# Kernel tuning notes

Measured on AMD Instinct MI355X. Metric: run time of the kernel, lower is better.

Reference implementation:

```python
import jax, jax.numpy as jnp
import numpy as np

H = 768       # hidden size
NH = 12       # num attention heads
DH = H // NH  # head dim = 64
B = 32
S = 512


def setup_inputs() -> dict:
    key = jax.random.key(0)
    ks = jax.random.split(key, 7)
    scale = 1.0 / np.sqrt(H)
    return {
        "inputs": jax.random.normal(ks[0], (B, S, H), dtype=jnp.float32),
        "Wq": jax.random.normal(ks[1], (H, H), dtype=jnp.float32) * scale,
        "bq": jnp.zeros((H,), dtype=jnp.float32),
        "Wk": jax.random.normal(ks[2], (H, H), dtype=jnp.float32) * scale,
        "bk": jnp.zeros((H,), dtype=jnp.float32),
        "Wv": jax.random.normal(ks[3], (H, H), dtype=jnp.float32) * scale,
        "bv": jnp.zeros((H,), dtype=jnp.float32),
    }


def reference(inputs, Wq, bq, Wk, bk, Wv, bv):
    # BertSelfAttention: linear projections (torch Linear: x @ W.T + b)
    def split_heads(x):  # [B,S,H] -> [B,NH,S,DH]
        return x.reshape(B, S, NH, DH).transpose(0, 2, 1, 3)

    q = split_heads(inputs @ Wq.T + bq)
    k = split_heads(inputs @ Wk.T + bk)
    v = split_heads(inputs @ Wv.T + bv)

    # scores [B,NH,S,S]; the wrapper adds an all-zero attention mask (no-op)
    scores = jnp.einsum("bhqd,bhkd->bhqk", q, k) / jnp.sqrt(jnp.float32(DH))
    probs = jax.nn.softmax(scores, axis=-1)
    ctx = jnp.einsum("bhqk,bhkd->bhqd", probs, v)  # [B,NH,S,DH]
    ctx = ctx.transpose(0, 2, 1, 3).reshape(B, S, H)
    return jnp.tanh(ctx)
```

## Files before the change

kernel.cpp:

```cpp
#include <hip/hip_runtime.h>
#include <hip/hip_bf16.h>
#include <cmath>

#define Bc   32
#define Sc_  512
#define Hc   768
#define NHc  12
#define DHc  64
#define Mc   (Bc * Sc_)
#define Ntot (3 * Hc)

#define QSCALE 0.18033688011112042f

typedef __attribute__((ext_vector_type(8))) short short8v;
typedef __attribute__((ext_vector_type(8))) unsigned short ushort8v;
typedef __attribute__((ext_vector_type(4))) float f32x4;

static __device__ __forceinline__ ushort f2b(float f) {
    __hip_bfloat16 h = __float2bfloat16(f);
    return *reinterpret_cast<ushort*>(&h);
}

static __device__ __forceinline__ void gl2lds(const ushort* g, ushort* l) {
    __builtin_amdgcn_global_load_lds(
        (const __attribute__((address_space(1))) unsigned int*)g,
        (__attribute__((address_space(3))) unsigned int*)l, 16, 0, 0);
}

static __device__ __forceinline__ float fast_tanh(float x) {
    float e = __builtin_amdgcn_exp2f(x * 2.885390081777927f);
    return 1.0f - 2.0f * __builtin_amdgcn_rcpf(e + 1.0f);
}

#define NXC (Mc * 96)
#define NWC (Ntot * 96)
__global__ __launch_bounds__(256) void convert_pack(
    const float* __restrict__ X,
    const float* __restrict__ Wq, const float* __restrict__ Wk,
    const float* __restrict__ Wv,
    const float* __restrict__ bq, const float* __restrict__ bk,
    const float* __restrict__ bv,
    ushort* __restrict__ Xt, ushort* __restrict__ Wt, float* __restrict__ bbp)
{
    int tid = blockIdx.x * 256 + threadIdx.x;
    if (tid < NXC) {
        int kc   = tid % 96;
        int m    = tid / 96;
        int mblk = m >> 7, mrow = m & 127;
        const float* src = X + (size_t)m * Hc + kc * 8;
        float4 f0 = *(const float4*)&src[0];
        float4 f1 = *(const float4*)&src[4];
        ushort8v o;
        o[0] = f2b(f0.x); o[1] = f2b(f0.y); o[2] = f2b(f0.z); o[3] = f2b(f0.w);
        o[4] = f2b(f1.x); o[5] = f2b(f1.y); o[6] = f2b(f1.z); o[7] = f2b(f1.w);
        *(ushort8v*)&Xt[((size_t)(mblk * 96 + kc)) * 1024 + mrow * 8] = o;
    } else if (tid < NXC + NWC) {
        int t2 = tid - NXC;
        int kc   = t2 % 96;
        int n    = t2 / 96;
        int nblk = n >> 7, nrow = n & 127;
        int z = n / Hc, nn = n - z * Hc;
        const float* W = (z == 0) ? Wq : (z == 1) ? Wk : Wv;
        const float* src = W + (size_t)nn * Hc + kc * 8;
        float4 f0 = *(const float4*)&src[0];
        float4 f1 = *(const float4*)&src[4];
        ushort8v o;
        o[0] = f2b(f0.x); o[1] = f2b(f0.y); o[2] = f2b(f0.z); o[3] = f2b(f0.w);
        o[4] = f2b(f1.x); o[5] = f2b(f1.y); o[6] = f2b(f1.z); o[7] = f2b(f1.w);
        *(ushort8v*)&Wt[((size_t)(nblk * 96 + kc)) * 1024 + nrow * 8] = o;
    } else if (tid < NXC + NWC + Ntot) {
        int i = tid - NXC - NWC;
        int z = i / Hc, nn = i - z * Hc;
        bbp[i] = ((z == 0) ? bq : (z == 1) ? bk : bv)[nn];
    }
}

__global__ __launch_bounds__(256) void qkv_mfma(
    const ushort* __restrict__ Xt, const ushort* __restrict__ Wt,
    const float* __restrict__ bbp,
    ushort* __restrict__ Qb, ushort* __restrict__ Kt, ushort* __restrict__ Vt)
{
    const int tid = threadIdx.x;
    const int wave = tid >> 6, lane = tid & 63;
    const int quad = lane >> 4, l16 = lane & 15;
    const int wr = wave >> 1, wc = wave & 1;
    const int m0 = blockIdx.x * 128;
    const int n0 = blockIdx.y * 128;

    __shared__ __align__(16) ushort As[4096];
    __shared__ __align__(16) ushort Bs[4096];

    f32x4 acc[4][4];
    #pragma unroll
    for (int i = 0; i < 4; ++i)
        #pragma unroll
        for (int j = 0; j < 4; ++j) acc[i][j] = (f32x4)(0.f);

    const ushort* gA = Xt + (size_t)blockIdx.x * (96 * 1024) + wave * 1024 + lane * 8;
    const ushort* gB = Wt + (size_t)blockIdx.y * (96 * 1024) + wave * 1024 + lane * 8;
    ushort* lA = As + wave * 1024;
    ushort* lB = Bs + wave * 1024;

    for (int t = 0; t < 24; ++t) {
        const ushort* ga = gA + t * 4096;
        const ushort* gb = gB + t * 4096;
        gl2lds(ga,       lA);
        gl2lds(ga + 512, lA + 512);
        gl2lds(gb,       lB);
        gl2lds(gb + 512, lB + 512);
        __syncthreads();

        short8v a[4], b[4];
        #pragma unroll
        for (int i = 0; i < 4; ++i)
            a[i] = *(const short8v*)&As[quad * 1024 + (wr * 64 + i * 16 + l16) * 8];
        #pragma unroll
        for (int j = 0; j < 4; ++j)
            b[j] = *(const short8v*)&Bs[quad * 1024 + (wc * 64 + j * 16 + l16) * 8];
        #pragma unroll
        for (int i = 0; i < 4; ++i)
            #pragma unroll
            for (int j = 0; j < 4; ++j)
                acc[i][j] = __builtin_amdgcn_mfma_f32_16x16x32_bf16(
                    a[i], b[j], acc[i][j], 0, 0, 0);
        __syncthreads();
    }

    const int z = n0 / Hc;
    #pragma unroll
    for (int j = 0; j < 4; ++j) {
        const int n  = n0 + wc * 64 + j * 16 + l16;
        const int nn = n - z * Hc;
        const int h  = nn >> 6, d = nn & 63;
        const float bias = bbp[n];
        #pragma unroll
        for (int i = 0; i < 4; ++i) {
            const int mbase = m0 + wr * 64 + i * 16 + quad * 4;
            const int bb = mbase >> 9;
            const int s0 = mbase & 511;
            const size_t head = (size_t)(bb * NHc + h) * (Sc_ * DHc);
            if (z == 0) {
                size_t base = head + (size_t)s0 * DHc + d;
                #pragma unroll
                for (int r = 0; r < 4; ++r)
                    Qb[base + (size_t)r * DHc] = f2b((acc[i][j][r] + bias) * QSCALE);
            } else if (z == 1) {
                size_t base = head + (s0 >> 6) * 4096 + (d >> 3) * 512
                            + (s0 & 63) * 8 + (d & 7);
                #pragma unroll
                for (int r = 0; r < 4; ++r)
                    Kt[base + r * 8] = f2b(acc[i][j][r] + bias);
            } else {
                size_t base = head + (s0 >> 6) * 4096 + ((s0 & 63) >> 3) * 512
                            + d * 8 + (s0 & 7);
                ushort4 o;
                o.x = f2b(acc[i][j][0] + bias);
                o.y = f2b(acc[i][j][1] + bias);
                o.z = f2b(acc[i][j][2] + bias);
                o.w = f2b(acc[i][j][3] + bias);
                *(ushort4*)&Vt[base] = o;
            }
        }
    }
}

__global__ __launch_bounds__(256) void attn_mfma(
    const ushort* __restrict__ Qb, const ushort* __restrict__ Kt,
    const ushort* __restrict__ Vt, float* __restrict__ out)
{
    const int b = blockIdx.z, h = blockIdx.y;
    const int wave = threadIdx.x >> 6;
    const int lane = threadIdx.x & 63;
    const int quad = lane >> 4, l16 = lane & 15;
    const int q0 = blockIdx.x * 128 + wave * 32;
    const int sw = l16 & 7;

    const size_t head = (size_t)(b * NHc + h) * (Sc_ * DHc);
    const ushort* __restrict__ Q = Qb + head;
    const ushort* __restrict__ K = Kt + head;
    const ushort* __restrict__ V = Vt + head;

    __shared__ __align__(16) ushort Plds[4][2][1024];

    short8v aq[2][2];
    #pragma unroll
    for (int u = 0; u < 2; ++u)
        #pragma unroll
        for (int hf = 0; hf < 2; ++hf)
            aq[u][hf] = *(const short8v*)
                &Q[(size_t)(q0 + u * 16 + l16) * DHc + hf * 32 + quad * 8];

    f32x4 o[2][4];
    #pragma unroll
    for (int u = 0; u < 2; ++u)
        #pragma unroll
        for (int t = 0; t < 4; ++t) o[u][t] = (f32x4)(0.f);
    float rs[2] = {0.f, 0.f};

    for (int kb = 0; kb < 8; ++kb) {
        const ushort* Kb_ = K + kb * 4096;
        const ushort* Vb_ = V + kb * 4096;

        short8v kf[4][2];
        #pragma unroll
        for (int t = 0; t < 4; ++t) {
            kf[t][0] = *(const short8v*)&Kb_[quad * 512 + (t * 16 + l16) * 8];
            kf[t][1] = *(const short8v*)&Kb_[(4 + quad) * 512 + (t * 16 + l16) * 8];
        }

        f32x4 sa[2][4];
        #pragma unroll
        for (int u = 0; u < 2; ++u)
            #pragma unroll
            for (int t = 0; t < 4; ++t) {
                f32x4 s = __builtin_amdgcn_mfma_f32_16x16x32_bf16(
                    kf[t][0], aq[u][0], (f32x4)(0.f), 0, 0, 0);
                sa[u][t] = __builtin_amdgcn_mfma_f32_16x16x32_bf16(
                    kf[t][1], aq[u][1], s, 0, 0, 0);
            }

        #pragma unroll
        for (int u = 0; u < 2; ++u) {
            #pragma unroll
            for (int t = 0; t < 4; ++t) {
                float p0 = __builtin_amdgcn_exp2f(sa[u][t][0]);
                float p1 = __builtin_amdgcn_exp2f(sa[u][t][1]);
                float p2 = __builtin_amdgcn_exp2f(sa[u][t][2]);
                float p3 = __builtin_amdgcn_exp2f(sa[u][t][3]);
                rs[u] += (p0 + p1) + (p2 + p3);
                ushort4 pk;
                pk.x = f2b(p0); pk.y = f2b(p1); pk.z = f2b(p2); pk.w = f2b(p3);
                int c = t * 2 + (quad >> 1);
                int addr = l16 * 64 + ((c ^ sw) * 8) + (quad & 1) * 4;
                *(ushort4*)&Plds[wave][u][addr] = pk;
            }
        }

        short8v pa[2][2];
        #pragma unroll
        for (int u = 0; u < 2; ++u) {
            pa[u][0] = *(const short8v*)&Plds[wave][u][l16 * 64 + ((quad ^ sw) * 8)];
            pa[u][1] = *(const short8v*)&Plds[wave][u][l16 * 64 + (((4 + quad) ^ sw) * 8)];
        }

        #pragma unroll
        for (int t2 = 0; t2 < 4; ++t2) {
            short8v vf0 = *(const short8v*)&Vb_[quad * 512 + (t2 * 16 + l16) * 8];
            short8v vf1 = *(const short8v*)&Vb_[(4 + quad) * 512 + (t2 * 16 + l16) * 8];
            #pragma unroll
            for (int u = 0; u < 2; ++u) {
                o[u][t2] = __builtin_amdgcn_mfma_f32_16x16x32_bf16(
                    pa[u][0], vf0, o[u][t2], 0, 0, 0);
                o[u][t2] = __builtin_amdgcn_mfma_f32_16x16x32_bf16(
                    pa[u][1], vf1, o[u][t2], 0, 0, 0);
            }
        }
    }

    #pragma unroll
    for (int u = 0; u < 2; ++u) {
        float l = rs[u];
        l += __shfl_xor(l, 16);
        l += __shfl_xor(l, 32);
        #pragma unroll
        for (int r = 0; r < 4; ++r) {
            float lr = __shfl(l, quad * 4 + r);
            float inv = 1.0f / lr;
            int q = q0 + u * 16 + quad * 4 + r;
            size_t base = ((size_t)b * Sc_ + q) * Hc + h * DHc;
            #pragma unroll
            for (int t2 = 0; t2 < 4; ++t2)
                out[base + t2 * 16 + l16] = fast_tanh(o[u][t2][r] * inv);
        }
    }
}

extern "C" void kernel_launch(void* const* d_in, const int* in_sizes, int n_in,
                              void* d_out, int out_size, void* d_ws, size_t ws_size,
                              hipStream_t stream) {
    const float* X  = (const float*)d_in[0];
    const float* Wq = (const float*)d_in[1];
    const float* bq = (const float*)d_in[2];
    const float* Wk = (const float*)d_in[3];
    const float* bk = (const float*)d_in[4];
    const float* Wv = (const float*)d_in[5];
    const float* bv = (const float*)d_in[6];
    float* out = (float*)d_out;

    ushort* Qb  = (ushort*)d_ws;
    ushort* Kt  = Qb + (size_t)Mc * Hc;
    ushort* Vt  = Kt + (size_t)Mc * Hc;
    ushort* Xt  = Vt + (size_t)Mc * Hc;
    ushort* Wt  = Xt + (size_t)Mc * Hc;
    float*  bbp = (float*)(Wt + (size_t)Ntot * Hc);

    {
        int total = NXC + NWC + Ntot;
        convert_pack<<<(total + 255) / 256, 256, 0, stream>>>(
            X, Wq, Wk, Wv, bq, bk, bv, Xt, Wt, bbp);
    }

    dim3 g1(Mc / 128, Ntot / 128);
    qkv_mfma<<<g1, 256, 0, stream>>>(Xt, Wt, bbp, Qb, Kt, Vt);

    dim3 g2(Sc_ / 128, NHc, Bc);
    attn_mfma<<<g2, 256, 0, stream>>>(Qb, Kt, Vt, out);
}
```

Measured before the change: 237.1 us.

## Stage convert-pack through LDS for coalesced writes; remap attention grid for locality

The fp32-to-bf16 pack kernel now uses 128-row blocks. Each block converts 32-column slices into a shared-memory tile, then writes the packed blocked layout with contiguous 16-byte stores, instead of per-thread scattered stores. The attention launch becomes a 1D grid that groups the four query tiles of eight consecutive heads together, so blocks sharing K/V run close in time and can reuse them from cache. The packing kernel now has far fewer blocks and adds two barriers per pass, so it may expose less parallelism.

```diff
diff --git a/kernel.cpp b/kernel.cpp
--- a/kernel.cpp
+++ b/kernel.cpp
@@ -32,8 +32,6 @@
     return 1.0f - 2.0f * __builtin_amdgcn_rcpf(e + 1.0f);
 }
 
-#define NXC (Mc * 96)
-#define NWC (Ntot * 96)
 __global__ __launch_bounds__(256) void convert_pack(
     const float* __restrict__ X,
     const float* __restrict__ Wq, const float* __restrict__ Wk,
@@ -42,36 +40,66 @@
     const float* __restrict__ bv,
     ushort* __restrict__ Xt, ushort* __restrict__ Wt, float* __restrict__ bbp)
 {
-    int tid = blockIdx.x * 256 + threadIdx.x;
-    if (tid < NXC) {
-        int kc   = tid % 96;
-        int m    = tid / 96;
-        int mblk = m >> 7, mrow = m & 127;
-        const float* src = X + (size_t)m * Hc + kc * 8;
-        float4 f0 = *(const float4*)&src[0];
-        float4 f1 = *(const float4*)&src[4];
-        ushort8v o;
-        o[0] = f2b(f0.x); o[1] = f2b(f0.y); o[2] = f2b(f0.z); o[3] = f2b(f0.w);
-        o[4] = f2b(f1.x); o[5] = f2b(f1.y); o[6] = f2b(f1.z); o[7] = f2b(f1.w);
-        *(ushort8v*)&Xt[((size_t)(mblk * 96 + kc)) * 1024 + mrow * 8] = o;
-    } else if (tid < NXC + NWC) {
-        int t2 = tid - NXC;
-        int kc   = t2 % 96;
-        int n    = t2 / 96;
-        int nblk = n >> 7, nrow = n & 127;
-        int z = n / Hc, nn = n - z * Hc;
+    const int bx = blockIdx.x;
+    const int t  = threadIdx.x;
+
+    __shared__ ushort T[128 * 36];
+
+    const float* base;
+    ushort* out;
+    if (bx < 128) {
+        base = X + (size_t)bx * 128 * Hc;
+        out  = Xt + (size_t)bx * (96 * 1024);
+    } else {
+        int nblk = bx - 128;
+        int n0 = nblk * 128;
+        int z = n0 / Hc;
+        int nn0 = n0 - z * Hc;
         const float* W = (z == 0) ? Wq : (z == 1) ? Wk : Wv;
-        const float* src = W + (size_t)nn * Hc + kc * 8;
-        float4 f0 = *(const float4*)&src[0];
-        float4 f1 = *(const float4*)&src[4];
-        ushort8v o;
-        o[0] = f2b(f0.x); o[1] = f2b(f0.y); o[2] = f2b(f0.z); o[3] = f2b(f0.w);
-        o[4] = f2b(f1.x); o[5] = f2b(f1.y); o[6] = f2b(f1.z); o[7] = f2b(f1.w);
-        *(ushort8v*)&Wt[((size_t)(nblk * 96 + kc)) * 1024 + nrow * 8] = o;
-    } else if (tid < NXC + NWC + Ntot) {
-        int i = tid - NXC - NWC;
-        int z = i / Hc, nn = i - z * Hc;
-        bbp[i] = ((z == 0) ? bq : (z == 1) ? bk : bv)[nn];
+        base = W + (size_t)nn0 * Hc;
+        out  = Wt + (size_t)nblk * (96 * 1024);
+    }
+
+    const int row_r = t >> 1, half = t & 1;
+    const int row_w = t & 127, cb = t >> 7;
+
+    for (int pp = 0; pp < 4; ++pp) {
+        const int pass = blockIdx.y * 4 + pp;
+        const int k0 = pass * 32;
+        const float* p = base + (size_t)row_r * Hc + k0 + half * 16;
+        float4 f0 = *(const float4*)&p[0];
+        float4 f1 = *(const float4*)&p[4];
+        float4 f2 = *(const float4*)&p[8];
+        float4 f3 = *(const float4*)&p[12];
+        int wb = row_r * 36 + half * 16;
+        ushort4 u0, u1, u2, u3;
+        u0.x = f2b(f0.x); u0.y = f2b(f0.y); u0.z = f2b(f0.z); u0.w = f2b(f0.w);
+        u1.x = f2b(f1.x); u1.y = f2b(f1.y); u1.z = f2b(f1.z); u1.w = f2b(f1.w);
+        u2.x = f2b(f2.x); u2.y = f2b(f2.y); u2.z = f2b(f2.z); u2.w = f2b(f2.w);
+        u3.x = f2b(f3.x); u3.y = f2b(f3.y); u3.z = f2b(f3.z); u3.w = f2b(f3.w);
+        *(ushort4*)&T[wb + 0]  = u0;
+        *(ushort4*)&T[wb + 4]  = u1;
+        *(ushort4*)&T[wb + 8]  = u2;
+        *(ushort4*)&T[wb + 12] = u3;
+        __syncthreads();
+        #pragma unroll
+        for (int u = 0; u < 2; ++u) {
+            int c = cb * 2 + u;
+            ushort4 lo = *(const ushort4*)&T[row_w * 36 + c * 8];
+            ushort4 hi = *(const ushort4*)&T[row_w * 36 + c * 8 + 4];
+            ushort8v v;
+            *(ushort4*)&v = lo;
+            *((ushort4*)&v + 1) = hi;
+            *(ushort8v*)&out[(size_t)(pass * 4 + c) * 1024 + row_w * 8] = v;
+        }
+        __syncthreads();
+    }
+
+    if (bx == 0 && blockIdx.y == 0) {
+        for (int i = t; i < Ntot; i += 256) {
+            int z = i / Hc, nn = i - z * Hc;
+            bbp[i] = ((z == 0) ? bq : (z == 1) ? bk : bv)[nn];
+        }
     }
 }
 
@@ -168,14 +196,19 @@
     const ushort* __restrict__ Qb, const ushort* __restrict__ Kt,
     const ushort* __restrict__ Vt, float* __restrict__ out)
 {
-    const int b = blockIdx.z, h = blockIdx.y;
+    const int bid = blockIdx.x;
+    const int super = bid >> 5, l = bid & 31;
+    const int head_lin = super * 8 + (l & 7);
+    const int qt = l >> 3;
+    const int b = head_lin / NHc, h = head_lin % NHc;
+
     const int wave = threadIdx.x >> 6;
     const int lane = threadIdx.x & 63;
     const int quad = lane >> 4, l16 = lane & 15;
-    const int q0 = blockIdx.x * 128 + wave * 32;
+    const int q0 = qt * 128 + wave * 32;
     const int sw = l16 & 7;
 
-    const size_t head = (size_t)(b * NHc + h) * (Sc_ * DHc);
+    const size_t head = (size_t)head_lin * (Sc_ * DHc);
     const ushort* __restrict__ Q = Qb + head;
     const ushort* __restrict__ K = Kt + head;
     const ushort* __restrict__ V = Vt + head;
@@ -259,12 +292,12 @@
 
     #pragma unroll
     for (int u = 0; u < 2; ++u) {
-        float l = rs[u];
-        l += __shfl_xor(l, 16);
-        l += __shfl_xor(l, 32);
+        float l2 = rs[u];
+        l2 += __shfl_xor(l2, 16);
+        l2 += __shfl_xor(l2, 32);
         #pragma unroll
         for (int r = 0; r < 4; ++r) {
-            float lr = __shfl(l, quad * 4 + r);
+            float lr = __shfl(l2, quad * 4 + r);
             float inv = 1.0f / lr;
             int q = q0 + u * 16 + quad * 4 + r;
             size_t base = ((size_t)b * Sc_ + q) * Hc + h * DHc;
@@ -294,15 +327,11 @@
     ushort* Wt  = Xt + (size_t)Mc * Hc;
     float*  bbp = (float*)(Wt + (size_t)Ntot * Hc);
 
-    {
-        int total = NXC + NWC + Ntot;
-        convert_pack<<<(total + 255) / 256, 256, 0, stream>>>(
-            X, Wq, Wk, Wv, bq, bk, bv, Xt, Wt, bbp);
-    }
+    dim3 g0(146, 6);
+    convert_pack<<<g0, 256, 0, stream>>>(X, Wq, Wk, Wv, bq, bk, bv, Xt, Wt, bbp);
 
     dim3 g1(Mc / 128, Ntot / 128);
     qkv_mfma<<<g1, 256, 0, stream>>>(Xt, Wt, bbp, Qb, Kt, Vt);
 
-    dim3 g2(Sc_ / 128, NHc, Bc);
-    attn_mfma<<<g2, 256, 0, stream>>>(Qb, Kt, Vt, out);
-}
+    attn_mfma<<<dim3(1536), 256, 0, stream>>>(Qb, Kt, Vt, out);
+}
```

Result: faster. 224.9 us (-5.1%).
